# Kernel tuning notes

Hardware: AMD Instinct MI355X
Metric: run time of the kernel (lower is better)

The kernel has to match this reference:

```python
import jax, jax.numpy as jnp
import numpy as np

NUM_JOINTS = 24
V = 6890
# standard SMPL kinematic tree (parent of joint i); index 0 is the root
PARENTS = [-1, 0, 0, 0, 1, 2, 3, 4, 5, 6, 7, 8, 9, 9, 9, 12, 13, 14, 16, 17, 18, 19, 20, 21]


def rodrigues(r):
    """Axis-angle [.., 3] -> rotation matrices [.., 3, 3] (batched Rodrigues)."""
    angle = jnp.sqrt(jnp.sum(r * r, axis=-1, keepdims=True) + 1e-16)
    axis = r / angle
    c = jnp.cos(angle)[..., None]
    s = jnp.sin(angle)[..., None]
    x, y, z = axis[..., 0], axis[..., 1], axis[..., 2]
    zeros = jnp.zeros_like(x)
    K = jnp.stack([zeros, -z, y, z, zeros, -x, -y, x, zeros], axis=-1).reshape(r.shape[:-1] + (3, 3))
    outer = axis[..., :, None] * axis[..., None, :]
    eye = jnp.eye(3, dtype=r.dtype)
    return c * eye + (1.0 - c) * outer + s * K


def with_zeros(Rt):
    """[B,3,4] -> [B,4,4] homogeneous transform."""
    B = Rt.shape[0]
    bottom = jnp.broadcast_to(jnp.array([0.0, 0.0, 0.0, 1.0], Rt.dtype), (B, 1, 4))
    return jnp.concatenate([Rt, bottom], axis=1)


def setup_inputs() -> dict:
    key = jax.random.key(0)
    ks = jax.random.split(key, 8)
    B = 1024
    return {
        "pose": jax.random.normal(ks[0], (B, 72), jnp.float32) * 0.3,
        "betas": jax.random.normal(ks[1], (B, 10), jnp.float32),
        "trans": jax.random.normal(ks[2], (B, 3), jnp.float32),
        "v_template": jax.random.normal(ks[3], (V, 3), jnp.float32),
        "shapedirs": jax.random.normal(ks[4], (V, 3, 10), jnp.float32) * 0.01,
        "posedirs": jax.random.normal(ks[5], (V, 3, 207), jnp.float32) * 0.01,
        "J_regressor": jax.random.uniform(ks[6], (24, V), jnp.float32) / V,
        "weights": jax.random.uniform(ks[7], (V, 24), jnp.float32),
    }


def reference(pose, betas, trans, v_template, shapedirs, posedirs, J_regressor, weights):
    B = pose.shape[0]
    dt = pose.dtype
    # pose -> per-joint rotation matrices [B,24,3,3]
    rot = rodrigues(pose.reshape(B, NUM_JOINTS, 3))
    root_rot = rot[:, 0]
    # pose blendshape features: non-root rotations minus identity, flattened [B,207]
    pose_map = (rot[:, 1:] - jnp.eye(3, dtype=dt)).reshape(B, (NUM_JOINTS - 1) * 9)
    v_shaped = v_template[None] + jnp.einsum('vcs,bs->bvc', shapedirs, betas)   # [B,V,3]
    j = jnp.einsum('jv,bvc->bjc', J_regressor, v_shaped)                        # [B,24,3]
    naked = v_shaped + jnp.einsum('vcp,bp->bvc', posedirs, pose_map)            # [B,V,3]
    v_posed = naked  # th_offsets is None
    # forward kinematics along the fixed 24-joint tree
    results = [None] * NUM_JOINTS
    results[0] = with_zeros(jnp.concatenate([root_rot, j[:, 0, :, None]], axis=2))
    for i in range(1, NUM_JOINTS):
        p = PARENTS[i]
        rel = with_zeros(jnp.concatenate([rot[:, i], (j[:, i] - j[:, p])[:, :, None]], axis=2))
        results[i] = results[p] @ rel
    G = jnp.stack(results, axis=1)  # [B,24,4,4] global transforms
    # remove rest-pose joint locations: G_rel = G - pack(G @ [j;0])
    j_h = jnp.concatenate([j, jnp.zeros((B, NUM_JOINTS, 1), dt)], axis=-1)      # [B,24,4]
    tmp = jnp.einsum('bjpq,bjq->bjp', G, j_h)                                   # [B,24,4]
    G_rel = G - jnp.concatenate([jnp.zeros(G.shape[:-1] + (3,), dt), tmp[..., None]], axis=-1)
    # linear blend skinning
    T = jnp.einsum('bjpq,vj->bpqv', G_rel, weights)                              # [B,4,4,V]
    rest_h = jnp.concatenate(
        [v_posed.transpose(0, 2, 1), jnp.ones((B, 1, v_posed.shape[1]), dt)], axis=1)  # [B,4,V]
    verts = jnp.einsum('bpqv,bqv->bvp', T, rest_h)[:, :, :3]                     # [B,V,3]
    jtr = G[:, :, :3, 3]                                                         # [B,24,3]
    # scale=1.0, normalise=False
    verts = verts + trans[:, None]
    jtr = jtr + trans[:, None]
    return verts, jtr, v_posed, naked, G
```

## Files before the change

### kernel.cpp

```cpp
#include <hip/hip_runtime.h>
#include <math.h>

#define V_NUM 6890
#define NJ 24
#define KTOT 217
#define KP 256
#define M_DIM (V_NUM * 3)
#define MPAD 20736
#define VPAD 6912

typedef __attribute__((ext_vector_type(8))) short bf16x8;
typedef __attribute__((ext_vector_type(4))) float f32x4;

__constant__ int c_parents[NJ] = {-1,0,0,0,1,2,3,4,5,6,7,8,9,9,9,12,13,14,16,17,18,19,20,21};

__device__ __forceinline__ unsigned short f2bf(float x) {
  union { float f; unsigned int u; } v; v.f = x;
  unsigned int r = v.u + 0x7fffu + ((v.u >> 16) & 1u);
  return (unsigned short)(r >> 16);
}

#define GLOBAL_AS __attribute__((address_space(1)))
#define LDS_AS __attribute__((address_space(3)))
__device__ __forceinline__ void gl_lds16(const void* g, void* l) {
  __builtin_amdgcn_global_load_lds((const GLOBAL_AS unsigned int*)g,
                                   (LDS_AS unsigned int*)l, 16, 0, 0);
}

__global__ __launch_bounds__(256) void k_regress(
    const float* __restrict__ JR, const float* __restrict__ SD,
    const float* __restrict__ VT, float* __restrict__ JS, float* __restrict__ Jt) {
  int j = blockIdx.x;
  int tid = threadIdx.x;
  float part[33];
#pragma unroll
  for (int q = 0; q < 33; q++) part[q] = 0.f;
  for (int v = tid; v < V_NUM; v += 256) {
    float jr = JR[j * V_NUM + v];
#pragma unroll
    for (int cc = 0; cc < 3; cc++) {
      part[30 + cc] += jr * VT[v * 3 + cc];
#pragma unroll
      for (int ss = 0; ss < 10; ss++)
        part[cc * 10 + ss] += jr * SD[(v * 3 + cc) * 10 + ss];
    }
  }
  __shared__ float sm[33][4];
  int lane = tid & 63, wid = tid >> 6;
#pragma unroll
  for (int q = 0; q < 33; q++) {
    float x = part[q];
    for (int off = 32; off > 0; off >>= 1) x += __shfl_down(x, off);
    if (lane == 0) sm[q][wid] = x;
  }
  __syncthreads();
  if (tid < 33) {
    float s = sm[tid][0] + sm[tid][1] + sm[tid][2] + sm[tid][3];
    if (tid < 30) JS[j * 30 + tid] = s;
    else Jt[j * 3 + (tid - 30)] = s;
  }
}

__global__ __launch_bounds__(256) void k_convA(
    const float* __restrict__ SD, const float* __restrict__ PD,
    unsigned short* __restrict__ Abf) {
  int m = blockIdx.x;
  int k = threadIdx.x;
  float v = 0.f;
  if (m < M_DIM && k < KTOT)
    v = (k < 10) ? SD[(size_t)m * 10 + k] : PD[(size_t)m * 207 + (k - 10)];
  Abf[(size_t)m * KP + k] = f2bf(v);
}

__global__ __launch_bounds__(256) void k_convW(
    const float* __restrict__ W, unsigned short* __restrict__ Wbf) {
  int idx = blockIdx.x * 256 + threadIdx.x;
  if (idx >= VPAD * 32) return;
  int v = idx >> 5, k = idx & 31;
  Wbf[idx] = (v < V_NUM && k < NJ) ? f2bf(W[(size_t)v * NJ + k]) : (unsigned short)0;
}

__global__ __launch_bounds__(64) void k_batch(
    const float* __restrict__ pose, const float* __restrict__ betas,
    const float* __restrict__ trans, const float* __restrict__ JS,
    const float* __restrict__ Jt, unsigned short* __restrict__ Kcb,
    unsigned short* __restrict__ GrelP, float* __restrict__ outG,
    float* __restrict__ outJtr, int B) {
  int b = blockIdx.x;
  int lane = threadIdx.x;
  __shared__ float rotS[NJ][9];
  __shared__ float jS[NJ * 3];
  __shared__ float Gs[NJ][12];
  __shared__ float GrS[NJ][12];

  if (lane < NJ) {
    float rx = pose[b * 72 + lane * 3 + 0];
    float ry = pose[b * 72 + lane * 3 + 1];
    float rz = pose[b * 72 + lane * 3 + 2];
    float a2 = rx * rx + ry * ry + rz * rz + 1e-16f;
    float ang = sqrtf(a2);
    float inv = 1.f / ang;
    float ux = rx * inv, uy = ry * inv, uz = rz * inv;
    float c = cosf(ang), s = sinf(ang), ic = 1.f - c;
    float R[9];
    R[0] = c + ic * ux * ux;      R[1] = ic * ux * uy - s * uz; R[2] = ic * ux * uz + s * uy;
    R[3] = ic * uy * ux + s * uz; R[4] = c + ic * uy * uy;      R[5] = ic * uy * uz - s * ux;
    R[6] = ic * uz * ux - s * uy; R[7] = ic * uz * uy + s * ux; R[8] = c + ic * uz * uz;
#pragma unroll
    for (int k = 0; k < 9; k++) rotS[lane][k] = R[k];
    if (lane > 0) {
#pragma unroll
      for (int k = 0; k < 9; k++) {
        float iden = (k == 0 || k == 4 || k == 8) ? 1.f : 0.f;
        Kcb[(size_t)b * KP + 10 + (lane - 1) * 9 + k] = f2bf(R[k] - iden);
      }
    }
  }
  if (lane < 10) Kcb[(size_t)b * KP + lane] = f2bf(betas[b * 10 + lane]);
  if (lane < KP - KTOT) Kcb[(size_t)b * KP + KTOT + lane] = 0;

  __syncthreads();
  for (int idx = lane; idx < 72; idx += 64) {
    float s = Jt[idx];
#pragma unroll
    for (int ss = 0; ss < 10; ss++) s += JS[idx * 10 + ss] * betas[b * 10 + ss];
    jS[idx] = s;
  }
  __syncthreads();

  if (lane == 0) {
#pragma unroll
    for (int p = 0; p < 3; p++) {
      Gs[0][p * 4 + 0] = rotS[0][p * 3 + 0];
      Gs[0][p * 4 + 1] = rotS[0][p * 3 + 1];
      Gs[0][p * 4 + 2] = rotS[0][p * 3 + 2];
      Gs[0][p * 4 + 3] = jS[p];
    }
    for (int i = 1; i < NJ; i++) {
      int par = c_parents[i];
      float t0 = jS[i * 3 + 0] - jS[par * 3 + 0];
      float t1 = jS[i * 3 + 1] - jS[par * 3 + 1];
      float t2 = jS[i * 3 + 2] - jS[par * 3 + 2];
#pragma unroll
      for (int p = 0; p < 3; p++) {
        float rp0 = Gs[par][p * 4 + 0], rp1 = Gs[par][p * 4 + 1], rp2 = Gs[par][p * 4 + 2];
#pragma unroll
        for (int q = 0; q < 3; q++) {
          Gs[i][p * 4 + q] = rp0 * rotS[i][0 * 3 + q] + rp1 * rotS[i][1 * 3 + q] + rp2 * rotS[i][2 * 3 + q];
        }
        Gs[i][p * 4 + 3] = rp0 * t0 + rp1 * t1 + rp2 * t2 + Gs[par][p * 4 + 3];
      }
    }
    for (int i = 0; i < NJ; i++) {
      float jx = jS[i * 3 + 0], jy = jS[i * 3 + 1], jz = jS[i * 3 + 2];
#pragma unroll
      for (int p = 0; p < 3; p++) {
        float g0 = Gs[i][p * 4 + 0], g1 = Gs[i][p * 4 + 1], g2 = Gs[i][p * 4 + 2];
        GrS[i][p * 4 + 0] = g0;
        GrS[i][p * 4 + 1] = g1;
        GrS[i][p * 4 + 2] = g2;
        GrS[i][p * 4 + 3] = Gs[i][p * 4 + 3] - (g0 * jx + g1 * jy + g2 * jz);
      }
    }
  }
  __syncthreads();

  for (int idx = lane; idx < NJ * 16; idx += 64) {
    int jj = idx >> 4, rc = idx & 15, p = rc >> 2, q = rc & 3;
    float val = (p < 3) ? Gs[jj][p * 4 + q] : ((q == 3) ? 1.f : 0.f);
    outG[(size_t)b * NJ * 16 + idx] = val;
  }
  for (int idx = lane; idx < NJ * 3; idx += 64) {
    int jj = idx / 3, p = idx % 3;
    outJtr[(size_t)b * NJ * 3 + idx] = Gs[jj][p * 4 + 3] + trans[b * 3 + p];
  }
  for (int idx = lane; idx < 16 * 40; idx += 64) {
    int c = idx / 40, j = idx % 40;
    GrelP[(size_t)b * 640 + idx] = (c < 12 && j < NJ) ? f2bf(GrS[j][c]) : (unsigned short)0;
  }
}

__global__ __launch_bounds__(256) void k_pose_mfma(
    const unsigned short* __restrict__ Kcb, const unsigned short* __restrict__ Abf,
    const float* __restrict__ VT, float* __restrict__ outVP, int B) {
  __shared__ char ldsraw[32768];
  __shared__ float vtS[128];
  unsigned short* At = (unsigned short*)ldsraw;
  unsigned short* Bt = At + 128 * 64;
  float* stage = (float*)ldsraw;

  const int tid = threadIdx.x;
  const int lane = tid & 63;
  const int w = tid >> 6;
  const int wr = w >> 1, wc = w & 1;
  const int b0 = blockIdx.y * 128;
  const int m0 = blockIdx.x * 128;

  if (tid < 128) vtS[tid] = (m0 + tid < M_DIM) ? VT[m0 + tid] : 0.f;

  f32x4 acc[4][4];
#pragma unroll
  for (int i = 0; i < 4; i++)
#pragma unroll
    for (int j = 0; j < 4; j++) acc[i][j] = (f32x4){0.f, 0.f, 0.f, 0.f};

  int Lrow[4], Lkb[4];
#pragma unroll
  for (int i = 0; i < 4; i++) {
    int L = w * 4096 + i * 1024 + lane * 16;
    int row = L >> 7;
    int kb = (L & 127) ^ ((row & 7) << 4);
    Lrow[i] = row;
    Lkb[i] = kb >> 1;
  }

  for (int kt = 0; kt < KP / 64; ++kt) {
#pragma unroll
    for (int i = 0; i < 4; i++) {
      const unsigned short* gA = Kcb + (size_t)(b0 + Lrow[i]) * KP + kt * 64 + Lkb[i];
      gl_lds16(gA, (char*)At + w * 4096 + i * 1024);
    }
#pragma unroll
    for (int i = 0; i < 4; i++) {
      const unsigned short* gB = Abf + (size_t)(m0 + Lrow[i]) * KP + kt * 64 + Lkb[i];
      gl_lds16(gB, (char*)Bt + w * 4096 + i * 1024);
    }
    __syncthreads();

#pragma unroll
    for (int h = 0; h < 2; ++h) {
      bf16x8 fm[4], fb[4];
#pragma unroll
      for (int fi = 0; fi < 4; fi++) {
        int row = wr * 64 + fi * 16 + (lane & 15);
        int byte = (row << 7) + ((h * 64 + ((lane >> 4) << 4)) ^ ((row & 7) << 4));
        fm[fi] = *(const bf16x8*)((const char*)Bt + byte);
      }
#pragma unroll
      for (int fj = 0; fj < 4; fj++) {
        int row = wc * 64 + fj * 16 + (lane & 15);
        int byte = (row << 7) + ((h * 64 + ((lane >> 4) << 4)) ^ ((row & 7) << 4));
        fb[fj] = *(const bf16x8*)((const char*)At + byte);
      }
#pragma unroll
      for (int fi = 0; fi < 4; fi++)
#pragma unroll
        for (int fj = 0; fj < 4; fj++)
          acc[fi][fj] = __builtin_amdgcn_mfma_f32_16x16x32_bf16(fm[fi], fb[fj], acc[fi][fj], 0, 0, 0);
    }
    __syncthreads();
  }

#pragma unroll
  for (int pp = 0; pp < 4; pp++) {
    __syncthreads();
    {
      int rowIdx = wc * 16 + (lane & 15);
#pragma unroll
      for (int fi = 0; fi < 4; fi++) {
        int ml = wr * 64 + fi * 16 + ((lane >> 4) << 2);
        *(f32x4*)&stage[rowIdx * 132 + ml] = acc[fi][pp];
      }
    }
    __syncthreads();
    int row = tid >> 3;
    int brow = ((row >> 4) * 64) + pp * 16 + (row & 15);
    size_t gb = (size_t)(b0 + brow) * M_DIM;
#pragma unroll
    for (int i = 0; i < 4; i++) {
      int col4 = (tid & 7) + 8 * i;
      int mg = m0 + col4 * 4;
      f32x4 v = *(f32x4*)&stage[row * 132 + col4 * 4];
      f32x4 vt = *(f32x4*)&vtS[col4 * 4];
      v = v + vt;
      if (mg + 3 < M_DIM) {
        *(f32x4*)(outVP + gb + mg) = v;
      } else {
#pragma unroll
        for (int r = 0; r < 4; r++)
          if (mg + r < M_DIM) outVP[gb + mg + r] = v[r];
      }
    }
  }
}

__global__ __launch_bounds__(256) void k_skin5(
    const float* __restrict__ VP, const unsigned short* __restrict__ Wbf,
    const unsigned short* __restrict__ GrelP, const float* __restrict__ trans,
    float* __restrict__ outNK, float* __restrict__ outVerts, int B) {
  __shared__ float Tl[4][64 * 13];
  const int tid = threadIdx.x;
  const int lane = tid & 63;
  const int w = tid >> 6;
  const int vl16 = lane & 15;
  const int p = lane >> 4;
  const int kb = p * 8;
  const int vbase = blockIdx.x * 256 + w * 64;
  const int b0 = blockIdx.y * 8;
  const int vg = vbase + lane;
  const bool vok = vg < V_NUM;

  bf16x8 wf[4];
#pragma unroll
  for (int sub = 0; sub < 4; sub++)
    wf[sub] = *(const bf16x8*)(Wbf + (size_t)(vbase + sub * 16 + vl16) * 32 + kb);

  float* myT = Tl[w];

  bf16x8 af = *(const bf16x8*)(GrelP + (size_t)b0 * 640 + vl16 * 40 + kb);
  float xc0 = 0.f, xc1 = 0.f, xc2 = 0.f;
  if (vok) {
    const float* xp = VP + (size_t)b0 * M_DIM + (size_t)vg * 3;
    xc0 = xp[0]; xc1 = xp[1]; xc2 = xp[2];
  }

#pragma unroll
  for (int bi = 0; bi < 8; bi++) {
    int b = b0 + bi;
    f32x4 acc[4];
#pragma unroll
    for (int sub = 0; sub < 4; sub++) {
      f32x4 z = (f32x4){0.f, 0.f, 0.f, 0.f};
      acc[sub] = __builtin_amdgcn_mfma_f32_16x16x32_bf16(af, wf[sub], z, 0, 0, 0);
    }
    if (p < 3) {
#pragma unroll
      for (int sub = 0; sub < 4; sub++) {
        int vi = sub * 16 + vl16;
#pragma unroll
        for (int r = 0; r < 4; r++)
          myT[vi * 13 + p * 4 + r] = acc[sub][r];
      }
    }
    bf16x8 af_n = af;
    float xn0 = 0.f, xn1 = 0.f, xn2 = 0.f;
    if (bi < 7) {
      af_n = *(const bf16x8*)(GrelP + (size_t)(b + 1) * 640 + vl16 * 40 + kb);
      if (vok) {
        const float* xp = VP + (size_t)(b + 1) * M_DIM + (size_t)vg * 3;
        xn0 = xp[0]; xn1 = xp[1]; xn2 = xp[2];
      }
    }
    asm volatile("s_waitcnt lgkmcnt(0)" ::: "memory");
    __builtin_amdgcn_sched_barrier(0);
    if (vok) {
      float t[12];
#pragma unroll
      for (int c = 0; c < 12; c++) t[c] = myT[lane * 13 + c];
      size_t base = (size_t)b * M_DIM + (size_t)vg * 3;
      float* onk = outNK + base;
      onk[0] = xc0; onk[1] = xc1; onk[2] = xc2;
      float* op = outVerts + base;
      op[0] = t[0] * xc0 + t[1] * xc1 + t[2] * xc2 + t[3] + trans[b * 3 + 0];
      op[1] = t[4] * xc0 + t[5] * xc1 + t[6] * xc2 + t[7] + trans[b * 3 + 1];
      op[2] = t[8] * xc0 + t[9] * xc1 + t[10] * xc2 + t[11] + trans[b * 3 + 2];
    }
    af = af_n; xc0 = xn0; xc1 = xn1; xc2 = xn2;
  }
}

extern "C" void kernel_launch(void* const* d_in, const int* in_sizes, int n_in,
                              void* d_out, int out_size, void* d_ws, size_t ws_size,
                              hipStream_t stream) {
  const float* pose  = (const float*)d_in[0];
  const float* betas = (const float*)d_in[1];
  const float* trans = (const float*)d_in[2];
  const float* vt    = (const float*)d_in[3];
  const float* sd    = (const float*)d_in[4];
  const float* pd    = (const float*)d_in[5];
  const float* jreg  = (const float*)d_in[6];
  const float* wgt   = (const float*)d_in[7];
  int B = in_sizes[0] / 72;

  float* out = (float*)d_out;
  size_t nvb = (size_t)B * M_DIM;
  float* o_verts = out;
  float* o_jtr   = o_verts + nvb;
  float* o_vp    = o_jtr + (size_t)B * NJ * 3;
  float* o_nk    = o_vp + nvb;
  float* o_G     = o_nk + nvb;

  char* wsb = (char*)d_ws;
  float* JS = (float*)wsb;
  float* Jt = JS + 720;
  size_t off = (720 + 72) * 4;
  unsigned short* Kcb   = (unsigned short*)(wsb + off);
  unsigned short* Abf   = (unsigned short*)(wsb + off + (size_t)B * KP * 2);
  unsigned short* GrelP = Abf + (size_t)MPAD * KP;
  unsigned short* Wbf   = GrelP + (size_t)B * 640;

  k_regress<<<24, 256, 0, stream>>>(jreg, sd, vt, JS, Jt);
  k_convA<<<MPAD, 256, 0, stream>>>(sd, pd, Abf);
  k_convW<<<(VPAD * 32 + 255) / 256, 256, 0, stream>>>(wgt, Wbf);
  k_batch<<<B, 64, 0, stream>>>(pose, betas, trans, JS, Jt, Kcb, GrelP, o_G, o_jtr, B);
  dim3 gC(MPAD / 128, B / 128);
  k_pose_mfma<<<gC, 256, 0, stream>>>(Kcb, Abf, vt, o_vp, B);
  dim3 gD(VPAD / 256, B / 8);
  k_skin5<<<gD, 256, 0, stream>>>(o_vp, Wbf, GrelP, trans, o_nk, o_verts, B);
}
```

Measured before the change: 151.7 us.

## Double-buffer pose GEMM LDS, merge conversion kernels, preload skin GrelP fragments

Fuses the two weight-conversion kernels into one launch to cut launch overhead. Double-buffers the LDS tiles in the pose-blend MFMA GEMM so the next K tile's global-to-LDS copy overlaps the current tile's MFMAs. The skin kernel now preloads all eight batch GrelP fragments up front and drops the explicit lgkmcnt wait and sched barrier. The doubled 64KB LDS footprint may reduce occupancy, and removing the explicit wait relies on compiler-inserted waits for LDS ordering.

```diff
diff --git a/kernel.cpp b/kernel.cpp
--- a/kernel.cpp
+++ b/kernel.cpp
@@ -61,23 +61,25 @@
   }
 }
 
-__global__ __launch_bounds__(256) void k_convA(
+__global__ __launch_bounds__(256) void k_conv(
     const float* __restrict__ SD, const float* __restrict__ PD,
-    unsigned short* __restrict__ Abf) {
-  int m = blockIdx.x;
-  int k = threadIdx.x;
-  float v = 0.f;
-  if (m < M_DIM && k < KTOT)
-    v = (k < 10) ? SD[(size_t)m * 10 + k] : PD[(size_t)m * 207 + (k - 10)];
-  Abf[(size_t)m * KP + k] = f2bf(v);
-}
-
-__global__ __launch_bounds__(256) void k_convW(
-    const float* __restrict__ W, unsigned short* __restrict__ Wbf) {
-  int idx = blockIdx.x * 256 + threadIdx.x;
-  if (idx >= VPAD * 32) return;
-  int v = idx >> 5, k = idx & 31;
-  Wbf[idx] = (v < V_NUM && k < NJ) ? f2bf(W[(size_t)v * NJ + k]) : (unsigned short)0;
+    const float* __restrict__ W,
+    unsigned short* __restrict__ Abf, unsigned short* __restrict__ Wbf) {
+  int bid = blockIdx.x;
+  int tid = threadIdx.x;
+  if (bid < MPAD) {
+    int m = bid, k = tid;
+    float v = 0.f;
+    if (m < M_DIM && k < KTOT)
+      v = (k < 10) ? SD[(size_t)m * 10 + k] : PD[(size_t)m * 207 + (k - 10)];
+    Abf[(size_t)m * KP + k] = f2bf(v);
+  } else {
+    int idx = (bid - MPAD) * 256 + tid;
+    if (idx < VPAD * 32) {
+      int v = idx >> 5, k = idx & 31;
+      Wbf[idx] = (v < V_NUM && k < NJ) ? f2bf(W[(size_t)v * NJ + k]) : (unsigned short)0;
+    }
+  }
 }
 
 __global__ __launch_bounds__(64) void k_batch(
@@ -183,11 +185,9 @@
 __global__ __launch_bounds__(256) void k_pose_mfma(
     const unsigned short* __restrict__ Kcb, const unsigned short* __restrict__ Abf,
     const float* __restrict__ VT, float* __restrict__ outVP, int B) {
-  __shared__ char ldsraw[32768];
-  __shared__ float vtS[128];
-  unsigned short* At = (unsigned short*)ldsraw;
-  unsigned short* Bt = At + 128 * 64;
+  __shared__ char ldsraw[65536];
   float* stage = (float*)ldsraw;
+  float* vtS   = (float*)(ldsraw + 17408);
 
   const int tid = threadIdx.x;
   const int lane = tid & 63;
@@ -196,8 +196,6 @@
   const int b0 = blockIdx.y * 128;
   const int m0 = blockIdx.x * 128;
 
-  if (tid < 128) vtS[tid] = (m0 + tid < M_DIM) ? VT[m0 + tid] : 0.f;
-
   f32x4 acc[4][4];
 #pragma unroll
   for (int i = 0; i < 4; i++)
@@ -214,19 +212,28 @@
     Lkb[i] = kb >> 1;
   }
 
-  for (int kt = 0; kt < KP / 64; ++kt) {
-#pragma unroll
-    for (int i = 0; i < 4; i++) {
-      const unsigned short* gA = Kcb + (size_t)(b0 + Lrow[i]) * KP + kt * 64 + Lkb[i];
-      gl_lds16(gA, (char*)At + w * 4096 + i * 1024);
-    }
-#pragma unroll
-    for (int i = 0; i < 4; i++) {
-      const unsigned short* gB = Abf + (size_t)(m0 + Lrow[i]) * KP + kt * 64 + Lkb[i];
-      gl_lds16(gB, (char*)Bt + w * 4096 + i * 1024);
-    }
-    __syncthreads();
-
+#define STAGE(kt, c)                                                              \
+  {                                                                               \
+    char* bufA = ldsraw + (c) * 32768;                                            \
+    char* bufB = bufA + 16384;                                                    \
+    _Pragma("unroll")                                                             \
+    for (int i = 0; i < 4; i++) {                                                 \
+      const unsigned short* gA = Kcb + (size_t)(b0 + Lrow[i]) * KP + (kt) * 64 + Lkb[i]; \
+      gl_lds16(gA, bufA + w * 4096 + i * 1024);                                   \
+      const unsigned short* gB = Abf + (size_t)(m0 + Lrow[i]) * KP + (kt) * 64 + Lkb[i]; \
+      gl_lds16(gB, bufB + w * 4096 + i * 1024);                                   \
+    }                                                                             \
+  }
+
+  STAGE(0, 0);
+  __syncthreads();
+
+#pragma unroll
+  for (int kt = 0; kt < 4; ++kt) {
+    int cur = kt & 1;
+    if (kt < 3) STAGE(kt + 1, cur ^ 1);
+    const char* At = ldsraw + cur * 32768;
+    const char* Bt = At + 16384;
 #pragma unroll
     for (int h = 0; h < 2; ++h) {
       bf16x8 fm[4], fb[4];
@@ -234,13 +241,13 @@
       for (int fi = 0; fi < 4; fi++) {
         int row = wr * 64 + fi * 16 + (lane & 15);
         int byte = (row << 7) + ((h * 64 + ((lane >> 4) << 4)) ^ ((row & 7) << 4));
-        fm[fi] = *(const bf16x8*)((const char*)Bt + byte);
+        fm[fi] = *(const bf16x8*)(Bt + byte);
       }
 #pragma unroll
       for (int fj = 0; fj < 4; fj++) {
         int row = wc * 64 + fj * 16 + (lane & 15);
         int byte = (row << 7) + ((h * 64 + ((lane >> 4) << 4)) ^ ((row & 7) << 4));
-        fb[fj] = *(const bf16x8*)((const char*)At + byte);
+        fb[fj] = *(const bf16x8*)(At + byte);
       }
 #pragma unroll
       for (int fi = 0; fi < 4; fi++)
@@ -250,7 +257,9 @@
     }
     __syncthreads();
   }
-
+#undef STAGE
+
+  if (tid < 128) vtS[tid] = (m0 + tid < M_DIM) ? VT[m0 + tid] : 0.f;
 #pragma unroll
   for (int pp = 0; pp < 4; pp++) {
     __syncthreads();
@@ -284,7 +293,7 @@
   }
 }
 
-__global__ __launch_bounds__(256) void k_skin5(
+__global__ __launch_bounds__(256) void k_skin6(
     const float* __restrict__ VP, const unsigned short* __restrict__ Wbf,
     const unsigned short* __restrict__ GrelP, const float* __restrict__ trans,
     float* __restrict__ outNK, float* __restrict__ outVerts, int B) {
@@ -305,9 +314,13 @@
   for (int sub = 0; sub < 4; sub++)
     wf[sub] = *(const bf16x8*)(Wbf + (size_t)(vbase + sub * 16 + vl16) * 32 + kb);
 
+  bf16x8 af[8];
+#pragma unroll
+  for (int bi = 0; bi < 8; bi++)
+    af[bi] = *(const bf16x8*)(GrelP + (size_t)(b0 + bi) * 640 + vl16 * 40 + kb);
+
   float* myT = Tl[w];
 
-  bf16x8 af = *(const bf16x8*)(GrelP + (size_t)b0 * 640 + vl16 * 40 + kb);
   float xc0 = 0.f, xc1 = 0.f, xc2 = 0.f;
   if (vok) {
     const float* xp = VP + (size_t)b0 * M_DIM + (size_t)vg * 3;
@@ -321,7 +334,7 @@
 #pragma unroll
     for (int sub = 0; sub < 4; sub++) {
       f32x4 z = (f32x4){0.f, 0.f, 0.f, 0.f};
-      acc[sub] = __builtin_amdgcn_mfma_f32_16x16x32_bf16(af, wf[sub], z, 0, 0, 0);
+      acc[sub] = __builtin_amdgcn_mfma_f32_16x16x32_bf16(af[bi], wf[sub], z, 0, 0, 0);
     }
     if (p < 3) {
 #pragma unroll
@@ -332,30 +345,24 @@
           myT[vi * 13 + p * 4 + r] = acc[sub][r];
       }
     }
-    bf16x8 af_n = af;
     float xn0 = 0.f, xn1 = 0.f, xn2 = 0.f;
-    if (bi < 7) {
-      af_n = *(const bf16x8*)(GrelP + (size_t)(b + 1) * 640 + vl16 * 40 + kb);
-      if (vok) {
-        const float* xp = VP + (size_t)(b + 1) * M_DIM + (size_t)vg * 3;
-        xn0 = xp[0]; xn1 = xp[1]; xn2 = xp[2];
-      }
-    }
-    asm volatile("s_waitcnt lgkmcnt(0)" ::: "memory");
-    __builtin_amdgcn_sched_barrier(0);
+    if (bi < 7 && vok) {
+      const float* xp = VP + (size_t)(b + 1) * M_DIM + (size_t)vg * 3;
+      xn0 = xp[0]; xn1 = xp[1]; xn2 = xp[2];
+    }
     if (vok) {
-      float t[12];
-#pragma unroll
-      for (int c = 0; c < 12; c++) t[c] = myT[lane * 13 + c];
       size_t base = (size_t)b * M_DIM + (size_t)vg * 3;
       float* onk = outNK + base;
       onk[0] = xc0; onk[1] = xc1; onk[2] = xc2;
+      float t[12];
+#pragma unroll
+      for (int c = 0; c < 12; c++) t[c] = myT[lane * 13 + c];
       float* op = outVerts + base;
       op[0] = t[0] * xc0 + t[1] * xc1 + t[2] * xc2 + t[3] + trans[b * 3 + 0];
       op[1] = t[4] * xc0 + t[5] * xc1 + t[6] * xc2 + t[7] + trans[b * 3 + 1];
       op[2] = t[8] * xc0 + t[9] * xc1 + t[10] * xc2 + t[11] + trans[b * 3 + 2];
     }
-    af = af_n; xc0 = xn0; xc1 = xn1; xc2 = xn2;
+    xc0 = xn0; xc1 = xn1; xc2 = xn2;
   }
 }
 
@@ -390,11 +397,10 @@
   unsigned short* Wbf   = GrelP + (size_t)B * 640;
 
   k_regress<<<24, 256, 0, stream>>>(jreg, sd, vt, JS, Jt);
-  k_convA<<<MPAD, 256, 0, stream>>>(sd, pd, Abf);
-  k_convW<<<(VPAD * 32 + 255) / 256, 256, 0, stream>>>(wgt, Wbf);
+  k_conv<<<MPAD + (VPAD * 32 + 255) / 256, 256, 0, stream>>>(sd, pd, wgt, Abf, Wbf);
   k_batch<<<B, 64, 0, stream>>>(pose, betas, trans, JS, Jt, Kcb, GrelP, o_G, o_jtr, B);
   dim3 gC(MPAD / 128, B / 128);
   k_pose_mfma<<<gC, 256, 0, stream>>>(Kcb, Abf, vt, o_vp, B);
   dim3 gD(VPAD / 256, B / 8);
-  k_skin5<<<gD, 256, 0, stream>>>(o_vp, Wbf, GrelP, trans, o_nk, o_verts, B);
-}
+  k_skin6<<<gD, 256, 0, stream>>>(o_vp, Wbf, GrelP, trans, o_nk, o_verts, B);
+}
```

Result: no change. 151.4 us (-0.2%).
